# Kernel tuning notes

Measured on AMD Instinct MI355X. Metric: run time of the kernel, lower is better.

The kernel has to match this reference:

```python
import jax, jax.numpy as jnp
import numpy as np

WINDOW_SIZE = 5
SIGMA = 1.5


def gaussian_kernel_3d(size, sigma):
    # Faithful replication of the torch code (including its permute quirk):
    # kernel[i,j,k] = exp(-((k-off)^2 + (k-off)^2 + (i-off)^2) / (2*sigma^2))
    c = jnp.arange(size, dtype=jnp.float32) - size // 2
    ci = c[:, None, None]  # axis 0 term (from permute(2,0,1))
    ck = c[None, None, :]  # axis 2 term (coords and permute(1,0,2) coincide)
    g = jnp.exp(-(ck ** 2 + ck ** 2 + ci ** 2) / (2.0 * sigma ** 2))
    g = jnp.broadcast_to(g, (size, size, size))
    return g / g.sum()


def _conv3d(x, w, pad):
    # x: [N,C,D,H,W], w: [O,I,kd,kh,kw]
    return jax.lax.conv_general_dilated(
        x, w, window_strides=(1, 1, 1),
        padding=[(pad, pad)] * 3,
        dimension_numbers=('NCDHW', 'OIDHW', 'NCDHW'))


def setup_inputs() -> dict:
    key = jax.random.key(0)
    k1, k2 = jax.random.split(key)
    img1 = jax.random.uniform(k1, (4, 2, 128, 128, 128), dtype=jnp.float32)
    img2 = jax.random.uniform(k2, (4, 1, 128, 128, 128), dtype=jnp.float32)
    window = gaussian_kernel_3d(WINDOW_SIZE, SIGMA)[None, None]  # [1,1,5,5,5]
    return {"img1": img1, "img2": img2, "window": window}


def reference(img1, img2, window):
    ws = window.shape[-1]
    pad = ws // 2
    x1 = img1[:, 1:2]  # select channel 1, keep dim -> [B,1,D,H,W]
    x2 = img2
    mu1 = _conv3d(x1, window, pad)
    mu2 = _conv3d(x2, window, pad)
    mu1_sq = mu1 * mu1
    mu2_sq = mu2 * mu2
    mu1_mu2 = mu1 * mu2
    sigma1_sq = _conv3d(x1 * x1, window, pad) - mu1_sq
    sigma2_sq = _conv3d(x2 * x2, window, pad) - mu2_sq
    sigma12 = _conv3d(x1 * x2, window, pad) - mu1_mu2
    C1 = 0.01 ** 2
    C2 = 0.03 ** 2
    ssim_map = ((2.0 * mu1_mu2 + C1) * (2.0 * sigma12 + C2)) / (
        (mu1_sq + mu2_sq + C1) * (sigma1_sq + sigma2_sq + C2))
    return 1.0 - jnp.mean(ssim_map)
```

## Files before the change

### kernel.cpp

```cpp
#include <hip/hip_runtime.h>


#define NDIM 128
#define TH 4
#define WR (TH + 4)
#define DSUB 16
#define NHT (NDIM / TH)
#define NDT (NDIM / DSUB)
#define NB 4
#define NBLK (NHT * NDT * NB)

__global__ void factorize_window(const float* __restrict__ w, float* __restrict__ ws) {
    if (threadIdx.x == 0) {
        float w000 = w[0];
        #pragma unroll
        for (int i = 0; i < 5; ++i) ws[i]      = w[i * 25];
        #pragma unroll
        for (int j = 0; j < 5; ++j) ws[5 + j]  = w[j * 5] / w000;
        #pragma unroll
        for (int k = 0; k < 5; ++k) ws[10 + k] = w[k] / w000;
    }
}

__launch_bounds__(256, 4)
__global__ void ssim_main(const float* __restrict__ img1,
                          const float* __restrict__ img2,
                          const float* __restrict__ wfac,
                          float* __restrict__ partials) {
    const int bid = blockIdx.x;
    const int th = bid % NHT;
    const int td = (bid / NHT) % NDT;
    const int b  = bid / (NHT * NDT);

    const int h0 = th * TH, d0 = td * DSUB;
    const float* __restrict__ x1 = img1 + (size_t)(b * 2 + 1) * NDIM * NDIM * NDIM;
    const float* __restrict__ x2 = img2 + (size_t)b * NDIM * NDIM * NDIM;

    float uW[5], vW[5], tW[5];
    #pragma unroll
    for (int i = 0; i < 5; ++i) { uW[i] = wfac[i]; vW[i] = wfac[5 + i]; tW[i] = wfac[10 + i]; }

    __shared__ float sWc[5][WR][NDIM];
    __shared__ float sRed[4];

    const int tid  = threadIdx.x;
    const int wv   = tid >> 6;
    const int lane = tid & 63;
    const int sc   = wv * 32;
    const int wrow = lane >> 3;
    const int wg   = lane & 7;
    const int c0   = sc + wg * 4;
    const int ghw  = h0 + wrow - 2;
    const int orow = lane >> 4;
    const int oc   = sc + (lane & 15) * 2;

    float2 ring[5][5];
    float2 accS = make_float2(0.f, 0.f);

#define PHASE(I, P) do {                                                       \
    const int i_ = (I);                                                        \
    const int d_ = d0 - 2 + i_;                                                \
    float4 A0 = make_float4(0,0,0,0), A1 = A0, A2 = A0;                        \
    float4 B0 = A0, B1 = A0, B2 = A0;                                          \
    if (((unsigned)d_ < NDIM) && ((unsigned)ghw < NDIM)) {                     \
        const float* __restrict__ r1_ = x1 + ((size_t)d_ * NDIM + ghw) * NDIM; \
        const float* __restrict__ r2_ = x2 + ((size_t)d_ * NDIM + ghw) * NDIM; \
        if (c0 > 0)   { A0 = *(const float4*)(r1_ + c0 - 4);                   \
                        B0 = *(const float4*)(r2_ + c0 - 4); }                 \
        A1 = *(const float4*)(r1_ + c0);                                       \
        B1 = *(const float4*)(r2_ + c0);                                       \
        if (c0 < 124) { A2 = *(const float4*)(r1_ + c0 + 4);                   \
                        B2 = *(const float4*)(r2_ + c0 + 4); }                 \
    }                                                                          \
    float ra[12] = {A0.x,A0.y,A0.z,A0.w, A1.x,A1.y,A1.z,A1.w,                  \
                    A2.x,A2.y,A2.z,A2.w};                                      \
    float rb[12] = {B0.x,B0.y,B0.z,B0.w, B1.x,B1.y,B1.z,B1.w,                  \
                    B2.x,B2.y,B2.z,B2.w};                                      \
    float m1v[4], m2v[4], q11v[4], q22v[4], q12v[4];                           \
    _Pragma("unroll")                                                          \
    for (int k_ = 0; k_ < 4; ++k_) {                                           \
        float m1_=0.f, m2_=0.f, q11_=0.f, q22_=0.f, q12_=0.f;                  \
        _Pragma("unroll")                                                      \
        for (int c_ = 0; c_ < 5; ++c_) {                                       \
            const float a_ = ra[k_ + c_ + 2], b_ = rb[k_ + c_ + 2];            \
            const float ta_ = tW[c_] * a_, tb_ = tW[c_] * b_;                  \
            m1_ += ta_; m2_ += tb_;                                            \
            q11_ += ta_ * a_; q22_ += tb_ * b_; q12_ += ta_ * b_;              \
        }                                                                      \
        m1v[k_]=m1_; m2v[k_]=m2_; q11v[k_]=q11_; q22v[k_]=q22_; q12v[k_]=q12_; \
    }                                                                          \
        \
    asm volatile("" ::: "memory");                                             \
    *(float4*)&sWc[0][wrow][c0] = make_float4(m1v[0],m1v[1],m1v[2],m1v[3]);    \
    *(float4*)&sWc[1][wrow][c0] = make_float4(m2v[0],m2v[1],m2v[2],m2v[3]);    \
    *(float4*)&sWc[2][wrow][c0] = make_float4(q11v[0],q11v[1],q11v[2],q11v[3]);\
    *(float4*)&sWc[3][wrow][c0] = make_float4(q22v[0],q22v[1],q22v[2],q22v[3]);\
    *(float4*)&sWc[4][wrow][c0] = make_float4(q12v[0],q12v[1],q12v[2],q12v[3]);\
    asm volatile("" ::: "memory");  \
    _Pragma("unroll")                                                          \
    for (int f_ = 0; f_ < 5; ++f_) {                                           \
        float2 F_ = make_float2(0.f, 0.f);                                     \
        _Pragma("unroll")                                                      \
        for (int r_ = 0; r_ < 5; ++r_) {                                       \
            const float2 wv_ = *(const float2*)&sWc[f_][orow + r_][oc];        \
            F_.x += vW[r_] * wv_.x;                                            \
            F_.y += vW[r_] * wv_.y;                                            \
        }                                                                      \
        ring[(P)][f_] = F_;                                                    \
    }                                                                          \
    if (i_ >= 4) {                                                             \
        float2 F0 = make_float2(0,0), F1 = F0, F2 = F0, F3 = F0, F4 = F0;      \
        _Pragma("unroll")                                                      \
        for (int j_ = 0; j_ < 5; ++j_) {                                       \
            const int s_ = ((P) + 1 + j_) % 5;                                 \
            const float uw_ = uW[j_];                                          \
            F0.x += uw_*ring[s_][0].x; F0.y += uw_*ring[s_][0].y;              \
            F1.x += uw_*ring[s_][1].x; F1.y += uw_*ring[s_][1].y;              \
            F2.x += uw_*ring[s_][2].x; F2.y += uw_*ring[s_][2].y;              \
            F3.x += uw_*ring[s_][3].x; F3.y += uw_*ring[s_][3].y;              \
            F4.x += uw_*ring[s_][4].x; F4.y += uw_*ring[s_][4].y;              \
        }                                                                      \
        {                                                                      \
            const float mu1 = F0.x, mu2 = F1.x;                                \
            const float m11 = mu1*mu1, m22 = mu2*mu2, m12 = mu1*mu2;           \
            const float num = (2.f*m12 + 1e-4f) * (2.f*(F4.x - m12) + 9e-4f);  \
            const float den = (m11 + m22 + 1e-4f) *                            \
                              ((F2.x - m11) + (F3.x - m22) + 9e-4f);           \
            accS.x += __fdividef(num, den);                                    \
        }                                                                      \
        {                                                                      \
            const float mu1 = F0.y, mu2 = F1.y;                                \
            const float m11 = mu1*mu1, m22 = mu2*mu2, m12 = mu1*mu2;           \
            const float num = (2.f*m12 + 1e-4f) * (2.f*(F4.y - m12) + 9e-4f);  \
            const float den = (m11 + m22 + 1e-4f) *                            \
                              ((F2.y - m11) + (F3.y - m22) + 9e-4f);           \
            accS.y += __fdividef(num, den);                                    \
        }                                                                      \
    }                                                                          \
} while (0)

    for (int io = 0; io < 4; ++io) {
        const int ib = io * 5;
        PHASE(ib + 0, 0);
        PHASE(ib + 1, 1);
        PHASE(ib + 2, 2);
        PHASE(ib + 3, 3);
        PHASE(ib + 4, 4);
    }
#undef PHASE

    float acc = accS.x + accS.y;
    #pragma unroll
    for (int off = 32; off > 0; off >>= 1)
        acc += __shfl_down(acc, off, 64);
    __syncthreads();
    if ((tid & 63) == 0) sRed[wv] = acc;
    __syncthreads();
    if (tid == 0) partials[bid] = sRed[0] + sRed[1] + sRed[2] + sRed[3];
}

__global__ void finalize_kernel(const float* __restrict__ partials, float* __restrict__ out) {
    const int tid = threadIdx.x;
    double s = 0.0;
    for (int i = tid; i < NBLK; i += 256) s += (double)partials[i];
    #pragma unroll
    for (int off = 32; off > 0; off >>= 1)
        s += __shfl_down(s, off, 64);
    __shared__ double sm[4];
    if ((tid & 63) == 0) sm[tid >> 6] = s;
    __syncthreads();
    if (tid == 0)
        out[0] = 1.0f - (float)((sm[0] + sm[1] + sm[2] + sm[3]) / (double)(4LL * 128 * 128 * 128));
}

extern "C" void kernel_launch(void* const* d_in, const int* in_sizes, int n_in,
                              void* d_out, int out_size, void* d_ws, size_t ws_size,
                              hipStream_t stream) {
    const float* img1 = (const float*)d_in[0];
    const float* img2 = (const float*)d_in[1];
    const float* win  = (const float*)d_in[2];
    float* out = (float*)d_out;
    float* ws  = (float*)d_ws;
    float* wfac     = ws;
    float* partials = ws + 16;

    hipLaunchKernelGGL(factorize_window, dim3(1), dim3(64), 0, stream, win, wfac);
    hipLaunchKernelGGL(ssim_main, dim3(NBLK), dim3(256), 0, stream, img1, img2, wfac, partials);
    hipLaunchKernelGGL(finalize_kernel, dim3(1), dim3(256), 0, stream, partials, out);
}
```

Baseline: 160.6 us.

## Split W dimension across two blocks to double grid size and occupancy

Each block now covers a 64-column half of the W dimension instead of all 128, which doubles the block count and halves the per-thread work (2 columns per thread instead of 4, one output instead of two). Shared memory per block is halved and launch bounds are raised to 8 blocks per CU to increase occupancy and latency hiding. The cost is more redundant halo loads along W, narrower float2 global loads, and lower arithmetic intensity per thread.

```diff
diff --git a/kernel.cpp b/kernel.cpp
--- a/kernel.cpp
+++ b/kernel.cpp
@@ -5,10 +5,12 @@
 #define TH 4
 #define WR (TH + 4)
 #define DSUB 16
+#define SW 64
+#define NSS (NDIM / SW)
 #define NHT (NDIM / TH)
 #define NDT (NDIM / DSUB)
 #define NB 4
-#define NBLK (NHT * NDT * NB)
+#define NBLK (NHT * NDT * NB * NSS)
 
 __global__ void factorize_window(const float* __restrict__ w, float* __restrict__ ws) {
     if (threadIdx.x == 0) {
@@ -22,17 +24,19 @@
     }
 }
 
-__launch_bounds__(256, 4)
+__launch_bounds__(256, 8)
 __global__ void ssim_main(const float* __restrict__ img1,
                           const float* __restrict__ img2,
                           const float* __restrict__ wfac,
                           float* __restrict__ partials) {
     const int bid = blockIdx.x;
-    const int th = bid % NHT;
-    const int td = (bid / NHT) % NDT;
-    const int b  = bid / (NHT * NDT);
+    const int ss  = bid & (NSS - 1);
+    const int idx = bid >> 1;
+    const int th  = idx & (NHT - 1);
+    const int td  = (idx >> 5) & (NDT - 1);
+    const int b   = idx >> 8;
 
-    const int h0 = th * TH, d0 = td * DSUB;
+    const int h0 = th * TH, d0 = td * DSUB, cs = ss * SW;
     const float* __restrict__ x1 = img1 + (size_t)(b * 2 + 1) * NDIM * NDIM * NDIM;
     const float* __restrict__ x2 = img2 + (size_t)b * NDIM * NDIM * NDIM;
 
@@ -40,102 +44,85 @@
     #pragma unroll
     for (int i = 0; i < 5; ++i) { uW[i] = wfac[i]; vW[i] = wfac[5 + i]; tW[i] = wfac[10 + i]; }
 
-    __shared__ float sWc[5][WR][NDIM];
+    __shared__ float sWc[5][WR][SW];
     __shared__ float sRed[4];
 
     const int tid  = threadIdx.x;
-    const int wv   = tid >> 6;
+    const int wvid = tid >> 6;
     const int lane = tid & 63;
-    const int sc   = wv * 32;
     const int wrow = lane >> 3;
     const int wg   = lane & 7;
-    const int c0   = sc + wg * 4;
+    const int c0b  = wvid * 16 + wg * 2;
+    const int c0g  = cs + c0b;
     const int ghw  = h0 + wrow - 2;
     const int orow = lane >> 4;
-    const int oc   = sc + (lane & 15) * 2;
+    const int ocb  = wvid * 16 + (lane & 15);
 
-    float2 ring[5][5];
-    float2 accS = make_float2(0.f, 0.f);
+    float ring[5][5];
+    float accS = 0.f;
 
 #define PHASE(I, P) do {                                                       \
     const int i_ = (I);                                                        \
     const int d_ = d0 - 2 + i_;                                                \
-    float4 A0 = make_float4(0,0,0,0), A1 = A0, A2 = A0;                        \
-    float4 B0 = A0, B1 = A0, B2 = A0;                                          \
+    float2 A0 = make_float2(0.f, 0.f), A1 = A0, A2 = A0;                       \
+    float2 B0 = A0, B1 = A0, B2 = A0;                                          \
     if (((unsigned)d_ < NDIM) && ((unsigned)ghw < NDIM)) {                     \
         const float* __restrict__ r1_ = x1 + ((size_t)d_ * NDIM + ghw) * NDIM; \
         const float* __restrict__ r2_ = x2 + ((size_t)d_ * NDIM + ghw) * NDIM; \
-        if (c0 > 0)   { A0 = *(const float4*)(r1_ + c0 - 4);                   \
-                        B0 = *(const float4*)(r2_ + c0 - 4); }                 \
-        A1 = *(const float4*)(r1_ + c0);                                       \
-        B1 = *(const float4*)(r2_ + c0);                                       \
-        if (c0 < 124) { A2 = *(const float4*)(r1_ + c0 + 4);                   \
-                        B2 = *(const float4*)(r2_ + c0 + 4); }                 \
+        if (c0g > 0)   { A0 = *(const float2*)(r1_ + c0g - 2);                 \
+                         B0 = *(const float2*)(r2_ + c0g - 2); }               \
+        A1 = *(const float2*)(r1_ + c0g);                                      \
+        B1 = *(const float2*)(r2_ + c0g);                                      \
+        if (c0g < 126) { A2 = *(const float2*)(r1_ + c0g + 2);                 \
+                         B2 = *(const float2*)(r2_ + c0g + 2); }               \
     }                                                                          \
-    float ra[12] = {A0.x,A0.y,A0.z,A0.w, A1.x,A1.y,A1.z,A1.w,                  \
-                    A2.x,A2.y,A2.z,A2.w};                                      \
-    float rb[12] = {B0.x,B0.y,B0.z,B0.w, B1.x,B1.y,B1.z,B1.w,                  \
-                    B2.x,B2.y,B2.z,B2.w};                                      \
-    float m1v[4], m2v[4], q11v[4], q22v[4], q12v[4];                           \
+    float ra[6] = {A0.x,A0.y, A1.x,A1.y, A2.x,A2.y};                           \
+    float rb[6] = {B0.x,B0.y, B1.x,B1.y, B2.x,B2.y};                           \
+    float m1v[2], m2v[2], q11v[2], q22v[2], q12v[2];                           \
     _Pragma("unroll")                                                          \
-    for (int k_ = 0; k_ < 4; ++k_) {                                           \
+    for (int k_ = 0; k_ < 2; ++k_) {                                           \
         float m1_=0.f, m2_=0.f, q11_=0.f, q22_=0.f, q12_=0.f;                  \
         _Pragma("unroll")                                                      \
         for (int c_ = 0; c_ < 5; ++c_) {                                       \
-            const float a_ = ra[k_ + c_ + 2], b_ = rb[k_ + c_ + 2];            \
+            const float a_ = ra[k_ + c_], b_ = rb[k_ + c_];                    \
             const float ta_ = tW[c_] * a_, tb_ = tW[c_] * b_;                  \
             m1_ += ta_; m2_ += tb_;                                            \
             q11_ += ta_ * a_; q22_ += tb_ * b_; q12_ += ta_ * b_;              \
         }                                                                      \
         m1v[k_]=m1_; m2v[k_]=m2_; q11v[k_]=q11_; q22v[k_]=q22_; q12v[k_]=q12_; \
     }                                                                          \
-        \
+                     \
     asm volatile("" ::: "memory");                                             \
-    *(float4*)&sWc[0][wrow][c0] = make_float4(m1v[0],m1v[1],m1v[2],m1v[3]);    \
-    *(float4*)&sWc[1][wrow][c0] = make_float4(m2v[0],m2v[1],m2v[2],m2v[3]);    \
-    *(float4*)&sWc[2][wrow][c0] = make_float4(q11v[0],q11v[1],q11v[2],q11v[3]);\
-    *(float4*)&sWc[3][wrow][c0] = make_float4(q22v[0],q22v[1],q22v[2],q22v[3]);\
-    *(float4*)&sWc[4][wrow][c0] = make_float4(q12v[0],q12v[1],q12v[2],q12v[3]);\
+    *(float2*)&sWc[0][wrow][c0b] = make_float2(m1v[0], m1v[1]);                \
+    *(float2*)&sWc[1][wrow][c0b] = make_float2(m2v[0], m2v[1]);                \
+    *(float2*)&sWc[2][wrow][c0b] = make_float2(q11v[0], q11v[1]);              \
+    *(float2*)&sWc[3][wrow][c0b] = make_float2(q22v[0], q22v[1]);              \
+    *(float2*)&sWc[4][wrow][c0b] = make_float2(q12v[0], q12v[1]);              \
     asm volatile("" ::: "memory");  \
     _Pragma("unroll")                                                          \
     for (int f_ = 0; f_ < 5; ++f_) {                                           \
-        float2 F_ = make_float2(0.f, 0.f);                                     \
+        float F_ = 0.f;                                                        \
         _Pragma("unroll")                                                      \
-        for (int r_ = 0; r_ < 5; ++r_) {                                       \
-            const float2 wv_ = *(const float2*)&sWc[f_][orow + r_][oc];        \
-            F_.x += vW[r_] * wv_.x;                                            \
-            F_.y += vW[r_] * wv_.y;                                            \
-        }                                                                      \
+        for (int r_ = 0; r_ < 5; ++r_)                                         \
+            F_ += vW[r_] * sWc[f_][orow + r_][ocb];                            \
         ring[(P)][f_] = F_;                                                    \
     }                                                                          \
     if (i_ >= 4) {                                                             \
-        float2 F0 = make_float2(0,0), F1 = F0, F2 = F0, F3 = F0, F4 = F0;      \
+        float F0 = 0.f, F1 = 0.f, F2 = 0.f, F3 = 0.f, F4 = 0.f;                \
         _Pragma("unroll")                                                      \
         for (int j_ = 0; j_ < 5; ++j_) {                                       \
             const int s_ = ((P) + 1 + j_) % 5;                                 \
             const float uw_ = uW[j_];                                          \
-            F0.x += uw_*ring[s_][0].x; F0.y += uw_*ring[s_][0].y;              \
-            F1.x += uw_*ring[s_][1].x; F1.y += uw_*ring[s_][1].y;              \
-            F2.x += uw_*ring[s_][2].x; F2.y += uw_*ring[s_][2].y;              \
-            F3.x += uw_*ring[s_][3].x; F3.y += uw_*ring[s_][3].y;              \
-            F4.x += uw_*ring[s_][4].x; F4.y += uw_*ring[s_][4].y;              \
+            F0 += uw_*ring[s_][0]; F1 += uw_*ring[s_][1];                      \
+            F2 += uw_*ring[s_][2]; F3 += uw_*ring[s_][3];                      \
+            F4 += uw_*ring[s_][4];                                             \
         }                                                                      \
-        {                                                                      \
-            const float mu1 = F0.x, mu2 = F1.x;                                \
-            const float m11 = mu1*mu1, m22 = mu2*mu2, m12 = mu1*mu2;           \
-            const float num = (2.f*m12 + 1e-4f) * (2.f*(F4.x - m12) + 9e-4f);  \
-            const float den = (m11 + m22 + 1e-4f) *                            \
-                              ((F2.x - m11) + (F3.x - m22) + 9e-4f);           \
-            accS.x += __fdividef(num, den);                                    \
-        }                                                                      \
-        {                                                                      \
-            const float mu1 = F0.y, mu2 = F1.y;                                \
-            const float m11 = mu1*mu1, m22 = mu2*mu2, m12 = mu1*mu2;           \
-            const float num = (2.f*m12 + 1e-4f) * (2.f*(F4.y - m12) + 9e-4f);  \
-            const float den = (m11 + m22 + 1e-4f) *                            \
-                              ((F2.y - m11) + (F3.y - m22) + 9e-4f);           \
-            accS.y += __fdividef(num, den);                                    \
-        }                                                                      \
+        const float mu1 = F0, mu2 = F1;                                        \
+        const float m11 = mu1*mu1, m22 = mu2*mu2, m12 = mu1*mu2;               \
+        const float num = (2.f*m12 + 1e-4f) * (2.f*(F4 - m12) + 9e-4f);        \
+        const float den = (m11 + m22 + 1e-4f) *                                \
+                          ((F2 - m11) + (F3 - m22) + 9e-4f);                   \
+        accS += __fdividef(num, den);                                          \
     }                                                                          \
 } while (0)
 
@@ -149,12 +136,12 @@
     }
 #undef PHASE
 
-    float acc = accS.x + accS.y;
+    float acc = accS;
     #pragma unroll
     for (int off = 32; off > 0; off >>= 1)
         acc += __shfl_down(acc, off, 64);
     __syncthreads();
-    if ((tid & 63) == 0) sRed[wv] = acc;
+    if (lane == 0) sRed[wvid] = acc;
     __syncthreads();
     if (tid == 0) partials[bid] = sRed[0] + sRed[1] + sRed[2] + sRed[3];
 }
```

New measurement: 626.6 us. 290% more time.
